# Kernel tuning notes

Hardware: AMD Instinct MI355X
Metric: run time of the kernel (lower is better)

## Reference

```python
import jax, jax.numpy as jnp
import numpy as np

B, T, K = 256, 512, 128          # batch, seq_len, n_tag
START, STOP = 126, 127           # tag2idx[START_TAG], tag2idx[STOP_TAG]
NEG = -10000.0                   # same constant the torch module uses


def setup_inputs() -> dict:
    key = jax.random.key(0)
    k1, k2, k3 = jax.random.split(key, 3)
    feats = jax.random.normal(k1, (B, T, K), dtype=jnp.float32)
    tags = jax.random.randint(k2, (B, T), 0, 126)  # never START/STOP
    # learned CRF transition matrix: trans[to, from]
    transitions = 0.1 * jax.random.normal(k3, (K, K), dtype=jnp.float32)
    transitions = transitions.at[START, :].set(NEG).at[:, STOP].set(NEG)
    return {"feats": feats, "tags": tags, "transitions": transitions}


def _forward_alg(feats, trans):
    """Batched CRF forward algorithm. feats [B,T,K] -> log Z [B]."""
    b = feats.shape[0]
    init = jnp.full((b, K), NEG, feats.dtype).at[:, START].set(0.0)

    def step(alpha, feat_t):
        # scores[b, to, from] = alpha[b, from] + trans[to, from]
        scores = alpha[:, None, :] + trans[None, :, :]
        alpha_new = jax.nn.logsumexp(scores, axis=-1) + feat_t
        return alpha_new, None

    alpha, _ = jax.lax.scan(step, init, jnp.swapaxes(feats, 0, 1))
    return jax.nn.logsumexp(alpha + trans[STOP][None, :], axis=-1)


def _score_sentence(feats, tags, trans):
    """Batched gold path score. feats [B,T,K], tags [B,T] -> [B]."""
    b = feats.shape[0]
    start_col = jnp.full((b, 1), START, tags.dtype)
    tags_ext = jnp.concatenate([start_col, tags], axis=1)      # [B,T+1]
    trans_sc = trans[tags_ext[:, 1:], tags_ext[:, :-1]].sum(axis=1)
    emit_sc = jnp.take_along_axis(feats, tags[..., None], axis=2)[..., 0].sum(axis=1)
    return trans_sc + emit_sc + trans[STOP, tags[:, -1]]


def _viterbi(feats, trans):
    """Batched Viterbi decode. Returns (path_score [B], path [B,T])."""
    b = feats.shape[0]
    init = jnp.full((b, K), NEG, feats.dtype).at[:, START].set(0.0)

    def step(alpha, feat_t):
        scores = alpha[:, None, :] + trans[None, :, :]   # [B,to,from]
        bptr = jnp.argmax(scores, axis=-1)               # [B,to]
        alpha_new = jnp.max(scores, axis=-1) + feat_t
        return alpha_new, bptr

    alpha, bptrs = jax.lax.scan(step, init, jnp.swapaxes(feats, 0, 1))
    term = alpha + trans[STOP][None, :]
    last_tag = jnp.argmax(term, axis=-1)                 # [B]
    path_score = jnp.max(term, axis=-1)

    def back(tag_t, bp_t):
        prev = jnp.take_along_axis(bp_t, tag_t[:, None], axis=1)[:, 0]
        return prev, tag_t

    _, path = jax.lax.scan(back, last_tag, bptrs, reverse=True)  # [T,B]
    return path_score, jnp.swapaxes(path, 0, 1)


def reference(feats, tags, transitions):
    log_z = _forward_alg(feats, transitions)             # forward_alg per sentence
    gold = _score_sentence(feats, tags, transitions)     # score_sentence
    path_score, pred = _viterbi(feats, transitions)      # viterbi_decode
    loss = jnp.sum(log_z - gold) / jnp.float32(feats.shape[0] * feats.shape[1])
    return loss, path_score, pred
```

## Files before the change

kernel.cpp:

```cpp
#include <hip/hip_runtime.h>
#include <cstdint>
#include <cstddef>

#define BB 256
#define TT 512
#define KK 128
#define START_TAG 126
#define STOP_TAG 127
#define NEGV (-10000.0f)
#define NINF (-__builtin_huge_valf())

template<int CTRL>
__device__ __forceinline__ float dppf(float v, float old) {
  return __int_as_float(__builtin_amdgcn_update_dpp(
      __float_as_int(old), __float_as_int(v), CTRL, 0xf, 0xf, false));
}
template<int CTRL>
__device__ __forceinline__ int dppi(int v, int old) {
  return __builtin_amdgcn_update_dpp(old, v, CTRL, 0xf, 0xf, false);
}
__device__ __forceinline__ float wave_max63(float x) {
  x = fmaxf(x, dppf<0x111>(x, NINF));
  x = fmaxf(x, dppf<0x112>(x, NINF));
  x = fmaxf(x, dppf<0x114>(x, NINF));
  x = fmaxf(x, dppf<0x118>(x, NINF));
  x = fmaxf(x, dppf<0x142>(x, NINF));
  x = fmaxf(x, dppf<0x143>(x, NINF));
  return x;
}
__device__ __forceinline__ float max3f(float a, float b, float c) {
  float d;
  asm("v_max3_f32 %0, %1, %2, %3" : "=v"(d) : "v"(a), "v"(b), "v"(c));
  return d;
}
__device__ __forceinline__ int paddr(int i) { return (i >> 5) * 36 + (i & 31); }

__global__ __launch_bounds__(768, 3) void crf768(
    const float* __restrict__ feats, const float* __restrict__ trans,
    const int* __restrict__ tags,
    float* __restrict__ pscore, int* __restrict__ lasttag,
    float* __restrict__ alphaS, float* __restrict__ gb)
{
  const int b = blockIdx.x;
  const int tid = threadIdx.x;
  const bool isv = tid < 512;
  const int lane = tid & 63;
  const int wv = tid >> 6;

  __shared__ __align__(16) float AV[2][144];
  __shared__ __align__(16) float P [2][144];
  __shared__ __align__(16) float pwm[4];
  __shared__ float vitm[8]; __shared__ int viti[8];
  __shared__ float reds[4]; __shared__ float redg[4];

  int myto, h;
  if (isv) { myto = tid >> 2; h = tid & 3; }
  else { int q = tid - 512; myto = q >> 1; h = q & 1; }

  float R[64];
  if (isv) {
    const float4* tr = (const float4*)(trans + (size_t)myto * KK + h * 32);
#pragma unroll
    for (int c = 0; c < 8; ++c) {
      float4 v = tr[c];
      R[4*c+0]=v.x; R[4*c+1]=v.y; R[4*c+2]=v.z; R[4*c+3]=v.w;
    }
  } else {
    const float4* tr = (const float4*)(trans + (size_t)myto * KK + h * 64);
#pragma unroll
    for (int c = 0; c < 16; ++c) {
      float4 v = tr[c];
      R[4*c+0]=__expf(v.x); R[4*c+1]=__expf(v.y);
      R[4*c+2]=__expf(v.z); R[4*c+3]=__expf(v.w);
    }
  }

  if (isv) { if (h == 0) AV[0][paddr(myto)] = (myto==START_TAG)?0.0f:NEGV; }
  else     { if (h == 0) P[0][paddr(myto)]  = (myto==START_TAG)?1.0f:0.0f; }
  __syncthreads();

  const float* fb = feats + (size_t)b * TT * KK + myto;
  float* aSb = alphaS + (size_t)b * TT * KK + myto;

  float M = 0.0f;
  float fcur = fb[0];
  float aLast = 0.0f, pvLast = 0.0f;
  int cur = 0;

  for (int t = 0; t < TT; ++t) {
    const int tn = (t + 1 < TT) ? t + 1 : t;
    float fnext = fb[(size_t)tn * KK];

    if (isv) {
      const float* Ac = &AV[cur][0];
      const int base = h * 36;
      float4 p = *(const float4*)&Ac[base];
      float m0 = fmaxf(p.x + R[0], p.y + R[1]);
      float m1 = fmaxf(p.z + R[2], p.w + R[3]);
#pragma unroll
      for (int c = 1; c < 8; ++c) {
        p = *(const float4*)&Ac[base + c * 4];
        m0 = max3f(m0, p.x + R[4*c+0], p.y + R[4*c+1]);
        m1 = max3f(m1, p.z + R[4*c+2], p.w + R[4*c+3]);
      }
      float m = fmaxf(m0, m1);
      m = fmaxf(m, dppf<0xB1>(m, m));
      m = fmaxf(m, dppf<0x4E>(m, m));
      float a = m + fcur;
      if (h == 0) {
        AV[cur ^ 1][paddr(myto)] = a;
        __builtin_nontemporal_store(a, &aSb[(size_t)t * KK]);
      }
      aLast = a;
    } else {
      float corr = 1.0f;
      if ((t & 3) == 0 && t) {
        float4 pw = *(const float4*)pwm;
        float pmax = fmaxf(fmaxf(pw.x, pw.y), fmaxf(pw.z, pw.w));
        M += __logf(pmax);
        corr = 1.0f / pmax;
      }
      const float* Pc = &P[cur][0];
      const int base = h * 72;
      float s0=0.f, s1=0.f, s2=0.f, s3=0.f;
#pragma unroll
      for (int c = 0; c < 16; ++c) {
        float4 p = *(const float4*)&Pc[base + (c>>3)*36 + (c&7)*4];
        s0 = fmaf(R[4*c+0], p.x, s0);
        s1 = fmaf(R[4*c+1], p.y, s1);
        s2 = fmaf(R[4*c+2], p.z, s2);
        s3 = fmaf(R[4*c+3], p.w, s3);
      }
      float s = (s0 + s1) + (s2 + s3);
      s = s + dppf<0xB1>(s, s);
      float ef = __expf(fcur);
      if ((t & 3) == 0 && t) ef *= corr;
      float pv = s * ef;
      if (h == 0) P[cur ^ 1][paddr(myto)] = pv;
      pvLast = pv;
      if ((t & 3) == 3) {
        float wm = wave_max63(pv);
        if (lane == 63) pwm[wv - 8] = wm;
      }
    }
    __syncthreads();
    cur ^= 1;
    fcur = fnext;
  }

  if (isv) {
    float term = aLast + trans[(size_t)STOP_TAG * KK + myto];
    float m = term; int i = myto;
#pragma unroll
    for (int off = 1; off < 64; off <<= 1) {
      float mo = __shfl_xor(m, off, 64);
      int   io = __shfl_xor(i, off, 64);
      if (mo > m || (mo == m && io < i)) { m = mo; i = io; }
    }
    if (lane == 0) { vitm[wv] = m; viti[wv] = i; }
  } else {
    float e = (h == 0) ? pvLast * __expf(trans[(size_t)STOP_TAG * KK + myto]) : 0.0f;
#pragma unroll
    for (int off = 1; off < 64; off <<= 1) e += __shfl_xor(e, off, 64);
    if (lane == 0) reds[wv - 8] = e;
    const int lt = tid - 512;
    const int* tg = tags + (size_t)b * TT;
    const float* fg = feats + (size_t)b * TT * KK;
    float g = 0.0f;
#pragma unroll
    for (int k2 = 0; k2 < 2; ++k2) {
      int t = lt + k2 * 256;
      int ct = tg[t];
      int pv2 = (t == 0) ? START_TAG : tg[t - 1];
      g += trans[(size_t)ct * KK + pv2] + fg[(size_t)t * KK + ct];
      if (t == TT - 1) g += trans[(size_t)STOP_TAG * KK + ct];
    }
#pragma unroll
    for (int off = 1; off < 64; off <<= 1) g += __shfl_xor(g, off, 64);
    if (lane == 0) redg[wv - 8] = g;
  }
  __syncthreads();
  if (tid == 0) {
    float m = vitm[0]; int i = viti[0];
#pragma unroll
    for (int w = 1; w < 8; ++w)
      if (vitm[w] > m || (vitm[w] == m && viti[w] < i)) { m = vitm[w]; i = viti[w]; }
    pscore[b] = m; lasttag[b] = i;
  }
  if (tid == 512) {
    float se = reds[0] + reds[1] + reds[2] + reds[3];
    float sg = redg[0] + redg[1] + redg[2] + redg[3];
    gb[b] = (M + __logf(se)) - sg;
  }
}

__global__ __launch_bounds__(64) void backtrace_loss(
    const float* __restrict__ alphaS, const float* __restrict__ trans,
    const int* __restrict__ lasttag, const float* __restrict__ gb,
    float* __restrict__ pred, float* __restrict__ loss_out)
{
  const int lane = threadIdx.x;
  if (blockIdx.x == BB) {
    float v = gb[lane] + gb[lane + 64] + gb[lane + 128] + gb[lane + 192];
#pragma unroll
    for (int off = 1; off < 64; off <<= 1) v += __shfl_xor(v, off, 64);
    if (lane == 0) loss_out[0] = v / (float)(BB * TT);
    return;
  }
  const int b = blockIdx.x;
  __shared__ float tl[KK * KK];
  {
    const float4* src = (const float4*)trans;
    float4* dst = (float4*)tl;
#pragma unroll
    for (int i = 0; i < (KK * KK / 4) / 64; ++i) dst[lane + i * 64] = src[lane + i * 64];
  }
  int tag = lasttag[b];
  if (lane == 0) pred[(size_t)b * TT + (TT - 1)] = (float)tag;
  const float* arow = alphaS + (size_t)b * TT * KK;

  float p0[8], p1[8];
#pragma unroll
  for (int j = 0; j < 8; ++j) {
    int r = TT - 2 - j;
    p0[j] = arow[(size_t)r * KK + lane];
    p1[j] = arow[(size_t)r * KK + 64 + lane];
  }
  __syncthreads();

  for (int rb = TT - 2; rb >= 0; rb -= 8) {
#pragma unroll
    for (int j = 0; j < 8; ++j) {
      int r = rb - j;
      if (r >= 0) {
        float x0 = p0[j] + tl[tag * KK + lane];
        float x1 = p1[j] + tl[tag * KK + 64 + lane];
        float m = fmaxf(x0, x1);
        float M = wave_max63(m);
        M = __int_as_float(__builtin_amdgcn_readlane(__float_as_int(M), 63));
        unsigned long long b0 = __ballot(x0 == M);
        unsigned long long b1 = __ballot(x1 == M);
        tag = b0 ? (int)__builtin_ctzll(b0) : 64 + (int)__builtin_ctzll(b1);
        if (lane == 0) pred[(size_t)b * TT + r] = (float)tag;
        int rp = r - 8;
        if (rp >= 0) {
          p0[j] = arow[(size_t)rp * KK + lane];
          p1[j] = arow[(size_t)rp * KK + 64 + lane];
        }
      }
    }
  }
}

__global__ __launch_bounds__(768) void crf_main_fb(
    const float* __restrict__ feats, const float* __restrict__ trans,
    float* __restrict__ logz, float* __restrict__ pscore,
    int* __restrict__ lasttag, uint8_t* __restrict__ bptr)
{
  const int b = blockIdx.x;
  const int tid = threadIdx.x;
  const bool is_fwd = tid < 256;
  const int lane = tid & 63;

  __shared__ __align__(16) float P[2][144];
  __shared__ __align__(16) float AV[2][144];
  __shared__ __align__(16) float redmF[2][4];
  __shared__ float reds[4];
  __shared__ float vitm[8];
  __shared__ int   viti[8];

  int myto, h;
  if (is_fwd) { myto = tid >> 1; h = tid & 1; }
  else { int q = tid - 256; myto = q >> 2; h = q & 3; }

  float R[64];
  if (is_fwd) {
    const float4* tr = (const float4*)(trans + (size_t)myto * KK + h * 64);
#pragma unroll
    for (int c = 0; c < 16; ++c) {
      float4 v = tr[c];
      R[4*c+0]=expf(v.x); R[4*c+1]=expf(v.y); R[4*c+2]=expf(v.z); R[4*c+3]=expf(v.w);
    }
  } else {
    const float4* tr = (const float4*)(trans + (size_t)myto * KK + h * 32);
#pragma unroll
    for (int c = 0; c < 8; ++c) {
      float4 v = tr[c];
      R[4*c+0]=v.x; R[4*c+1]=v.y; R[4*c+2]=v.z; R[4*c+3]=v.w;
    }
  }

  if (is_fwd) { if (h == 0) P[0][paddr(myto)] = (myto==START_TAG)?1.0f:0.0f; }
  else        { if (h == 0) AV[0][paddr(myto)] = (myto==START_TAG)?0.0f:NEGV; }
  if (tid < 4) redmF[1][tid] = 0.0f;
  __syncthreads();

  const float* fb = feats + (size_t)b * TT * KK + myto;
  uint8_t* bp = bptr + (size_t)b * TT * KK + myto;

  float fcur = fb[0];
  float Mprev = 0.0f;
  float aCarry = 0.0f;
  int cur = 0;

  for (int t = 0; t < TT; ++t) {
    const int tn = (t + 1 < TT) ? t + 1 : t;
    float fnext = fb[(size_t)tn * KK];
    const int rd = (t + 1) & 1, wr = t & 1;

    if (is_fwd) {
      float4 rv = *(const float4*)&redmF[rd][0];
      float M1 = fmaxf(fmaxf(rv.x, rv.y), fmaxf(rv.z, rv.w));
      const float* Pc = &P[cur][0];
      const int base = h * 72;
      float s0=0.f, s1=0.f, s2=0.f, s3=0.f;
#pragma unroll
      for (int c = 0; c < 16; ++c) {
        float4 p = *(const float4*)&Pc[base + (c>>3)*36 + (c&7)*4];
        s0 = fmaf(R[4*c+0], p.x, s0);
        s1 = fmaf(R[4*c+1], p.y, s1);
        s2 = fmaf(R[4*c+2], p.z, s2);
        s3 = fmaf(R[4*c+3], p.w, s3);
      }
      float s = (s0 + s1) + (s2 + s3);
      s = s + dppf<0xB1>(s, s);
      float a = Mprev + logf(s) + fcur;
      float wm = wave_max63(a);
      if (lane == 63) redmF[wr][tid >> 6] = wm;
      float pv = expf(a - M1);
      if (h == 0) P[cur ^ 1][paddr(myto)] = pv;
      Mprev = M1;
      aCarry = a;
    } else {
      const float* Ac = &AV[cur][0];
      const int base = h * 36;
      const int fb0 = h * 32;
      float4 p0 = *(const float4*)&Ac[base];
      float m0 = p0.x + R[0], m1 = p0.y + R[1], m2 = p0.z + R[2], m3 = p0.w + R[3];
      int i0 = fb0, i1 = fb0+1, i2 = fb0+2, i3 = fb0+3;
#pragma unroll
      for (int c = 1; c < 8; ++c) {
        float4 p = *(const float4*)&Ac[base + c*4];
        float v0 = p.x + R[4*c+0]; if (v0 > m0) { m0 = v0; i0 = fb0+4*c+0; }
        float v1 = p.y + R[4*c+1]; if (v1 > m1) { m1 = v1; i1 = fb0+4*c+1; }
        float v2 = p.z + R[4*c+2]; if (v2 > m2) { m2 = v2; i2 = fb0+4*c+2; }
        float v3 = p.w + R[4*c+3]; if (v3 > m3) { m3 = v3; i3 = fb0+4*c+3; }
      }
      float m = m0; int i = i0;
      if (m1 > m || (m1 == m && i1 < i)) { m = m1; i = i1; }
      if (m2 > m || (m2 == m && i2 < i)) { m = m2; i = i2; }
      if (m3 > m || (m3 == m && i3 < i)) { m = m3; i = i3; }
      { float mo = dppf<0xB1>(m, m); int io = dppi<0xB1>(i, i);
        if (mo > m || (mo == m && io < i)) { m = mo; i = io; } }
      { float mo = dppf<0x4E>(m, m); int io = dppi<0x4E>(i, i);
        if (mo > m || (mo == m && io < i)) { m = mo; i = io; } }
      float a = m + fcur;
      if (h == 0) { AV[cur ^ 1][paddr(myto)] = a; bp[(size_t)t * KK] = (uint8_t)i; }
      aCarry = a;
    }
    __syncthreads();
    cur ^= 1;
    fcur = fnext;
  }

  float tstop = trans[(size_t)STOP_TAG * KK + myto];
  float term = aCarry + tstop;
  float M = 0.0f;
  if (is_fwd) {
    float wm = wave_max63(term);
    if (lane == 63) redmF[0][tid >> 6] = wm;
  } else {
    float m = term; int i = myto;
#pragma unroll
    for (int off = 1; off < 64; off <<= 1) {
      float mo = __shfl_xor(m, off, 64);
      int   io = __shfl_xor(i, off, 64);
      if (mo > m || (mo == m && io < i)) { m = mo; i = io; }
    }
    if (lane == 0) { vitm[(tid>>6)-4] = m; viti[(tid>>6)-4] = i; }
  }
  __syncthreads();
  if (is_fwd) {
    float4 rv = *(const float4*)&redmF[0][0];
    M = fmaxf(fmaxf(rv.x, rv.y), fmaxf(rv.z, rv.w));
    float e = (h == 0) ? expf(term - M) : 0.0f;
#pragma unroll
    for (int off = 1; off < 64; off <<= 1) e += __shfl_xor(e, off, 64);
    if (lane == 0) reds[tid >> 6] = e;
  } else if (tid == 256) {
    float m = vitm[0]; int i = viti[0];
#pragma unroll
    for (int w = 1; w < 8; ++w)
      if (vitm[w] > m || (vitm[w] == m && viti[w] < i)) { m = vitm[w]; i = viti[w]; }
    pscore[b] = m; lasttag[b] = i;
  }
  __syncthreads();
  if (tid == 0) logz[b] = M + logf(reds[0] + reds[1] + reds[2] + reds[3]);
}

__global__ __launch_bounds__(256) void backtrace_kernel(
    const uint8_t* __restrict__ bptr, const int* __restrict__ lasttag,
    float* __restrict__ pred)
{
  const int b = blockIdx.x;
  const int tid = threadIdx.x;
  __shared__ __align__(16) uint8_t lb[(TT / 2) * KK];
  __shared__ int tagcarry;
  if (tid == 0) tagcarry = lasttag[b];

  for (int half = 1; half >= 0; --half) {
    __syncthreads();
    const float4* src = reinterpret_cast<const float4*>(
        bptr + ((size_t)b * TT + (size_t)half * (TT / 2)) * KK);
    float4* dst = reinterpret_cast<float4*>(lb);
    for (int i = tid; i < (TT / 2) * KK / 16; i += 256) dst[i] = src[i];
    __syncthreads();
    if (tid == 0) {
      int tag = tagcarry;
      for (int t = TT / 2 - 1; t >= 0; --t) {
        int gt = half * (TT / 2) + t;
        pred[(size_t)b * TT + gt] = (float)tag;
        tag = lb[t * KK + tag];
      }
      tagcarry = tag;
    }
  }
}

__global__ __launch_bounds__(64) void gold_kernel(
    const float* __restrict__ feats, const int* __restrict__ tags,
    const float* __restrict__ trans, const float* __restrict__ logz,
    float* __restrict__ gb)
{
  const int b = blockIdx.x;
  const int lane = threadIdx.x;
  const int* tg = tags + (size_t)b * TT;
  const float* fb = feats + (size_t)b * TT * KK;
  float g = 0.0f;
#pragma unroll
  for (int k = 0; k < TT / 64; ++k) {
    int t = lane * (TT / 64) + k;
    int ct = tg[t];
    int pv = (t == 0) ? START_TAG : tg[t - 1];
    g += trans[ct * KK + pv] + fb[(size_t)t * KK + ct];
  }
  if (lane == 63) g += trans[STOP_TAG * KK + tg[TT - 1]];
#pragma unroll
  for (int off = 1; off <= 32; off <<= 1) g += __shfl_xor(g, off, 64);
  if (lane == 0) gb[b] = logz[b] - g;
}

__global__ __launch_bounds__(256) void loss_reduce(
    const float* __restrict__ gb, float* __restrict__ out)
{
  const int tid = threadIdx.x;
  const int lane = tid & 63, wv = tid >> 6;
  float v = gb[tid];
#pragma unroll
  for (int off = 1; off <= 32; off <<= 1) v += __shfl_xor(v, off, 64);
  __shared__ float red[4];
  if (lane == 0) red[wv] = v;
  __syncthreads();
  if (tid == 0) out[0] = (red[0] + red[1] + red[2] + red[3]) / (float)(BB * TT);
}

extern "C" void kernel_launch(void* const* d_in, const int* in_sizes, int n_in,
                              void* d_out, int out_size, void* d_ws, size_t ws_size,
                              hipStream_t stream) {
  const float* feats = (const float*)d_in[0];
  const int*   tags  = (const int*)d_in[1];
  const float* trans = (const float*)d_in[2];

  float* out    = (float*)d_out;
  float* loss   = out;
  float* pscore = out + 1;
  float* pred   = out + 1 + BB;
  (void)in_sizes; (void)n_in; (void)out_size;

  const size_t alpha_bytes = (size_t)BB * TT * KK * sizeof(float);
  const bool cheap = ws_size >= alpha_bytes + 4096;

  if (cheap) {
    float* alphaS  = (float*)d_ws;
    char*  wsend   = (char*)d_ws + alpha_bytes;
    int*   lasttag = (int*)(wsend);
    float* gb      = (float*)(wsend + BB * sizeof(int));
    crf768<<<BB, 768, 0, stream>>>(feats, trans, tags, pscore, lasttag,
                                   alphaS, gb);
    backtrace_loss<<<BB + 1, 64, 0, stream>>>(alphaS, trans, lasttag, gb,
                                              pred, loss);
  } else {
    uint8_t* bptr    = (uint8_t*)d_ws;
    char*    wsend   = (char*)d_ws + (size_t)BB * TT * KK;
    float*   logz    = (float*)(wsend);
    int*     lasttag = (int*)(wsend + BB * sizeof(float));
    float*   gb      = (float*)(wsend + BB * sizeof(float) + BB * sizeof(int));
    crf_main_fb<<<BB, 768, 0, stream>>>(feats, trans, logz, pscore, lasttag, bptr);
    backtrace_kernel<<<BB, 256, 0, stream>>>(bptr, lasttag, pred);
    gold_kernel<<<BB, 64, 0, stream>>>(feats, tags, trans, logz, gb);
    loss_reduce<<<1, 256, 0, stream>>>(gb, loss);
  }
}
```

Before: 408.9 us.

## Widen CRF block to 1024 threads, splitting forward sum four ways

The forward-algorithm (sum-product) half of the block grows from 256 to 512 threads, so each target tag is split four ways like the Viterbi half. Each thread now does 8 float4 FMAs instead of 16 and adds one more DPP reduction step. Register arrays shrink to 32 entries, and the loop gets unroll 4. The final reductions now read the last alpha and P values from shared memory rather than per-thread registers. The risk is higher per-block thread and register pressure plus a more expensive barrier with 16 waves.

```diff
diff --git a/kernel.cpp b/kernel.cpp
--- a/kernel.cpp
+++ b/kernel.cpp
@@ -35,7 +35,7 @@
 }
 __device__ __forceinline__ int paddr(int i) { return (i >> 5) * 36 + (i & 31); }
 
-__global__ __launch_bounds__(768, 3) void crf768(
+__global__ __launch_bounds__(1024, 4) void crf1024(
     const float* __restrict__ feats, const float* __restrict__ trans,
     const int* __restrict__ tags,
     float* __restrict__ pscore, int* __restrict__ lasttag,
@@ -44,49 +44,42 @@
   const int b = blockIdx.x;
   const int tid = threadIdx.x;
   const bool isv = tid < 512;
+  const int q = isv ? tid : tid - 512;
+  const int to = q >> 2;
+  const int h  = q & 3;
   const int lane = tid & 63;
   const int wv = tid >> 6;
 
   __shared__ __align__(16) float AV[2][144];
   __shared__ __align__(16) float P [2][144];
-  __shared__ __align__(16) float pwm[4];
-  __shared__ float vitm[8]; __shared__ int viti[8];
-  __shared__ float reds[4]; __shared__ float redg[4];
-
-  int myto, h;
-  if (isv) { myto = tid >> 2; h = tid & 3; }
-  else { int q = tid - 512; myto = q >> 1; h = q & 1; }
-
-  float R[64];
-  if (isv) {
-    const float4* tr = (const float4*)(trans + (size_t)myto * KK + h * 32);
+  __shared__ __align__(16) float pwm[8];
+  __shared__ float vitm[2]; __shared__ int viti[2];
+  __shared__ float reds[2]; __shared__ float redg[8];
+
+  float R[32];
+  {
+    const float4* tr = (const float4*)(trans + (size_t)to * KK + h * 32);
 #pragma unroll
     for (int c = 0; c < 8; ++c) {
       float4 v = tr[c];
-      R[4*c+0]=v.x; R[4*c+1]=v.y; R[4*c+2]=v.z; R[4*c+3]=v.w;
-    }
-  } else {
-    const float4* tr = (const float4*)(trans + (size_t)myto * KK + h * 64);
-#pragma unroll
-    for (int c = 0; c < 16; ++c) {
-      float4 v = tr[c];
-      R[4*c+0]=__expf(v.x); R[4*c+1]=__expf(v.y);
-      R[4*c+2]=__expf(v.z); R[4*c+3]=__expf(v.w);
-    }
-  }
-
-  if (isv) { if (h == 0) AV[0][paddr(myto)] = (myto==START_TAG)?0.0f:NEGV; }
-  else     { if (h == 0) P[0][paddr(myto)]  = (myto==START_TAG)?1.0f:0.0f; }
-  __syncthreads();
-
-  const float* fb = feats + (size_t)b * TT * KK + myto;
-  float* aSb = alphaS + (size_t)b * TT * KK + myto;
+      if (isv) { R[4*c+0]=v.x; R[4*c+1]=v.y; R[4*c+2]=v.z; R[4*c+3]=v.w; }
+      else     { R[4*c+0]=__expf(v.x); R[4*c+1]=__expf(v.y);
+                 R[4*c+2]=__expf(v.z); R[4*c+3]=__expf(v.w); }
+    }
+  }
+
+  if (isv) { if (h == 0) AV[0][paddr(to)] = (to==START_TAG)?0.0f:NEGV; }
+  else     { if (h == 0) P[0][paddr(to)]  = (to==START_TAG)?1.0f:0.0f; }
+  __syncthreads();
+
+  const float* fb = feats + (size_t)b * TT * KK + to;
+  float* aSb = alphaS + (size_t)b * TT * KK + to;
 
   float M = 0.0f;
   float fcur = fb[0];
-  float aLast = 0.0f, pvLast = 0.0f;
   int cur = 0;
 
+#pragma unroll 4
   for (int t = 0; t < TT; ++t) {
     const int tn = (t + 1 < TT) ? t + 1 : t;
     float fnext = fb[(size_t)tn * KK];
@@ -106,26 +99,27 @@
       float m = fmaxf(m0, m1);
       m = fmaxf(m, dppf<0xB1>(m, m));
       m = fmaxf(m, dppf<0x4E>(m, m));
-      float a = m + fcur;
       if (h == 0) {
-        AV[cur ^ 1][paddr(myto)] = a;
+        float a = m + fcur;
+        AV[cur ^ 1][paddr(to)] = a;
         __builtin_nontemporal_store(a, &aSb[(size_t)t * KK]);
       }
-      aLast = a;
     } else {
       float corr = 1.0f;
       if ((t & 3) == 0 && t) {
-        float4 pw = *(const float4*)pwm;
-        float pmax = fmaxf(fmaxf(pw.x, pw.y), fmaxf(pw.z, pw.w));
+        float4 w0 = *(const float4*)&pwm[0];
+        float4 w1 = *(const float4*)&pwm[4];
+        float pmax = fmaxf(fmaxf(fmaxf(w0.x, w0.y), fmaxf(w0.z, w0.w)),
+                           fmaxf(fmaxf(w1.x, w1.y), fmaxf(w1.z, w1.w)));
         M += __logf(pmax);
         corr = 1.0f / pmax;
       }
       const float* Pc = &P[cur][0];
-      const int base = h * 72;
+      const int base = h * 36;
       float s0=0.f, s1=0.f, s2=0.f, s3=0.f;
 #pragma unroll
-      for (int c = 0; c < 16; ++c) {
-        float4 p = *(const float4*)&Pc[base + (c>>3)*36 + (c&7)*4];
+      for (int c = 0; c < 8; ++c) {
+        float4 p = *(const float4*)&Pc[base + c * 4];
         s0 = fmaf(R[4*c+0], p.x, s0);
         s1 = fmaf(R[4*c+1], p.y, s1);
         s2 = fmaf(R[4*c+2], p.z, s2);
@@ -133,11 +127,11 @@
       }
       float s = (s0 + s1) + (s2 + s3);
       s = s + dppf<0xB1>(s, s);
+      s = s + dppf<0x4E>(s, s);
       float ef = __expf(fcur);
       if ((t & 3) == 0 && t) ef *= corr;
       float pv = s * ef;
-      if (h == 0) P[cur ^ 1][paddr(myto)] = pv;
-      pvLast = pv;
+      if (h == 0) P[cur ^ 1][paddr(to)] = pv;
       if ((t & 3) == 3) {
         float wm = wave_max63(pv);
         if (lane == 63) pwm[wv - 8] = wm;
@@ -148,33 +142,31 @@
     fcur = fnext;
   }
 
-  if (isv) {
-    float term = aLast + trans[(size_t)STOP_TAG * KK + myto];
-    float m = term; int i = myto;
+  if (tid < KK) {
+    float term = AV[cur][paddr(tid)] + trans[(size_t)STOP_TAG * KK + tid];
+    float m = term; int i = tid;
 #pragma unroll
     for (int off = 1; off < 64; off <<= 1) {
       float mo = __shfl_xor(m, off, 64);
       int   io = __shfl_xor(i, off, 64);
       if (mo > m || (mo == m && io < i)) { m = mo; i = io; }
     }
-    if (lane == 0) { vitm[wv] = m; viti[wv] = i; }
-  } else {
-    float e = (h == 0) ? pvLast * __expf(trans[(size_t)STOP_TAG * KK + myto]) : 0.0f;
+    if (lane == 0) { vitm[tid >> 6] = m; viti[tid >> 6] = i; }
+  }
+  if (tid >= 512 && tid < 512 + KK) {
+    const int to2 = tid - 512;
+    float e = P[cur][paddr(to2)] * __expf(trans[(size_t)STOP_TAG * KK + to2]);
 #pragma unroll
     for (int off = 1; off < 64; off <<= 1) e += __shfl_xor(e, off, 64);
-    if (lane == 0) reds[wv - 8] = e;
-    const int lt = tid - 512;
+    if (lane == 0) reds[to2 >> 6] = e;
+  }
+  if (!isv) {
     const int* tg = tags + (size_t)b * TT;
     const float* fg = feats + (size_t)b * TT * KK;
-    float g = 0.0f;
-#pragma unroll
-    for (int k2 = 0; k2 < 2; ++k2) {
-      int t = lt + k2 * 256;
-      int ct = tg[t];
-      int pv2 = (t == 0) ? START_TAG : tg[t - 1];
-      g += trans[(size_t)ct * KK + pv2] + fg[(size_t)t * KK + ct];
-      if (t == TT - 1) g += trans[(size_t)STOP_TAG * KK + ct];
-    }
+    int ct = tg[q];
+    int pv2 = (q == 0) ? START_TAG : tg[q - 1];
+    float g = trans[(size_t)ct * KK + pv2] + fg[(size_t)q * KK + ct];
+    if (q == TT - 1) g += trans[(size_t)STOP_TAG * KK + ct];
 #pragma unroll
     for (int off = 1; off < 64; off <<= 1) g += __shfl_xor(g, off, 64);
     if (lane == 0) redg[wv - 8] = g;
@@ -182,15 +174,12 @@
   __syncthreads();
   if (tid == 0) {
     float m = vitm[0]; int i = viti[0];
-#pragma unroll
-    for (int w = 1; w < 8; ++w)
-      if (vitm[w] > m || (vitm[w] == m && viti[w] < i)) { m = vitm[w]; i = viti[w]; }
+    if (vitm[1] > m || (vitm[1] == m && viti[1] < i)) { m = vitm[1]; i = viti[1]; }
     pscore[b] = m; lasttag[b] = i;
   }
   if (tid == 512) {
-    float se = reds[0] + reds[1] + reds[2] + reds[3];
-    float sg = redg[0] + redg[1] + redg[2] + redg[3];
-    gb[b] = (M + __logf(se)) - sg;
+    float sg = redg[0]+redg[1]+redg[2]+redg[3]+redg[4]+redg[5]+redg[6]+redg[7];
+    gb[b] = (M + __logf(reds[0] + reds[1])) - sg;
   }
 }
 
@@ -485,8 +474,8 @@
     char*  wsend   = (char*)d_ws + alpha_bytes;
     int*   lasttag = (int*)(wsend);
     float* gb      = (float*)(wsend + BB * sizeof(int));
-    crf768<<<BB, 768, 0, stream>>>(feats, trans, tags, pscore, lasttag,
-                                   alphaS, gb);
+    crf1024<<<BB, 1024, 0, stream>>>(feats, trans, tags, pscore, lasttag,
+                                     alphaS, gb);
     backtrace_loss<<<BB + 1, 64, 0, stream>>>(alphaS, trans, lasttag, gb,
                                               pred, loss);
   } else {
```

Result: faster. 377.1 us (-7.8%).
